# Optimization experiments

Measured on AMD Instinct MI355X. Metric: run time of the kernel, lower is better.

## Reference

```python
import jax, jax.numpy as jnp
import numpy as np

SHAPE = (160, 160, 160)  # spatial grid (D, H, W)
N_VOX = 400_000
C_IN, C_OUT, K = 32, 64, 3


def setup_inputs() -> dict:
    key = jax.random.key(0)
    k1, k2, k3 = jax.random.split(key, 3)
    # unique active voxel coords (batch=0, z, y, x)
    rng = np.random.default_rng(0)
    flat = rng.choice(SHAPE[0] * SHAPE[1] * SHAPE[2], size=N_VOX, replace=False)
    z, y, x = np.unravel_index(flat, SHAPE)
    coors = np.stack([np.zeros(N_VOX, np.int32), z.astype(np.int32), y.astype(np.int32), x.astype(np.int32)], axis=1)
    features = jax.random.normal(k1, (N_VOX, C_IN), dtype=jnp.float32)
    weight = jax.random.normal(k2, (K * K * K, C_IN, C_OUT), dtype=jnp.float32) * (1.0 / np.sqrt(C_IN * K * K * K))
    bias = jax.random.normal(k3, (C_OUT,), dtype=jnp.float32) * 0.01
    return {"features": features, "coors": jnp.asarray(coors), "weight": weight, "bias": bias, "batch_size": 1}


def reference(features, coors, weight, bias, batch_size):
    # Submanifold sparse 3D conv: output coords == input coords.
    n = features.shape[0]
    b, z, y, x = coors[:, 0], coors[:, 1], coors[:, 2], coors[:, 3]
    D, H, W = SHAPE
    # dense voxel->row index lookup grid (the "hash map" for rulebook build)
    grid = jnp.full((batch_size, D, H, W), -1, dtype=jnp.int32)
    grid = grid.at[b, z, y, x].set(jnp.arange(n, dtype=jnp.int32))
    out = jnp.broadcast_to(bias, (n, C_OUT)).astype(features.dtype)
    k = 0
    for dz in (-1, 0, 1):
        for dy in (-1, 0, 1):
            for dx in (-1, 0, 1):
                nz, ny, nx = z + dz, y + dy, x + dx
                inb = (nz >= 0) & (nz < D) & (ny >= 0) & (ny < H) & (nx >= 0) & (nx < W)
                idx = grid[b, jnp.clip(nz, 0, D - 1), jnp.clip(ny, 0, H - 1), jnp.clip(nx, 0, W - 1)]
                valid = inb & (idx >= 0)
                gathered = jnp.where(valid[:, None], features[jnp.clip(idx, 0)], 0.0)  # [n, C_IN]
                out = out + gathered @ weight[k]  # small GEMM per kernel offset
                k += 1
    return out
```

## Files before the change

kernel.cpp:

```cpp
#include <hip/hip_runtime.h>
#include <stdint.h>

#define DD 160
#define HH 160
#define WW 160
#define NGRID (DD*HH*WW)
#define CIN 32
#define COUT 64
#define KK 27
#define BLOCK 1024
#define WPB 16
#define NBLOCKS 256
#define M27 0x07FFFFFFu

typedef _Float16 h2_t __attribute__((ext_vector_type(2)));

__device__ __forceinline__ h2_t as_h2(uint32_t u) {
    union { uint32_t u; h2_t h; } c; c.u = u; return c.h;
}
__device__ __forceinline__ uint32_t f2h(float f) {
    union { _Float16 h; uint16_t u; } c; c.h = (_Float16)f; return (uint32_t)c.u;
}

__device__ __forceinline__ float dot2(uint32_t fu, uint32_t wu, float acc) {
#if defined(__has_builtin)
#if __has_builtin(__builtin_amdgcn_fdot2)
    return __builtin_amdgcn_fdot2(as_h2(fu), as_h2(wu), acc, false);
#else
    h2_t f = as_h2(fu), w = as_h2(wu);
    acc = fmaf((float)f.x, (float)w.x, acc);
    return fmaf((float)f.y, (float)w.y, acc);
#endif
#else
    h2_t f = as_h2(fu), w = as_h2(wu);
    acc = fmaf((float)f.x, (float)w.x, acc);
    return fmaf((float)f.y, (float)w.y, acc);
#endif
}

__global__ void scatter_grid(const int4* __restrict__ coors, int* __restrict__ grid, int n) {
    int i = blockIdx.x * 256 + threadIdx.x;
    if (i < n) {
        int4 c = coors[i];
        grid[(c.y*HH + c.z)*WW + c.w] = i;
    }
}

__global__ void pack_weights(const float* __restrict__ w, uint4* __restrict__ wpk) {
    int t = blockIdx.x * 256 + threadIdx.x;
    if (t >= KK*4*COUT) return;
    int co = t & 63;
    int g  = (t >> 6) & 3;
    int k  = t >> 8;
    const float* base = w + (size_t)k*CIN*COUT + (size_t)(8*g)*COUT + co;
    uint4 r;
    r.x = f2h(base[0*COUT]) | (f2h(base[1*COUT]) << 16);
    r.y = f2h(base[2*COUT]) | (f2h(base[3*COUT]) << 16);
    r.z = f2h(base[4*COUT]) | (f2h(base[5*COUT]) << 16);
    r.w = f2h(base[6*COUT]) | (f2h(base[7*COUT]) << 16);
    wpk[t] = r;
}

__global__ void feats_to_h(const float4* __restrict__ f, uint2* __restrict__ o, int nq) {
    int i = blockIdx.x * 256 + threadIdx.x;
    if (i < nq) {
        float4 v = f[i];
        uint2 r;
        r.x = f2h(v.x) | (f2h(v.y) << 16);
        r.y = f2h(v.z) | (f2h(v.w) << 16);
        o[i] = r;
    }
}

#define LOAD4(D0,D1,D2,D3,kk) { \
    int j_ = __builtin_amdgcn_readlane(nidx, base + (kk)); \
    const uint4* fp_ = fh4 + (size_t)j_ * 4; \
    D0 = fp_[0]; D1 = fp_[1]; D2 = fp_[2]; D3 = fp_[3]; }

#define MAC4(F0,F1,F2,F3,kk) { \
    const uint4* wl_ = wlds + (size_t)(kk)*4*COUT + lane; \
    uint4 w0_ = wl_[0], w1_ = wl_[COUT], w2_ = wl_[2*COUT], w3_ = wl_[3*COUT]; \
    a0 = dot2(F0.x, w0_.x, a0); a1 = dot2(F0.y, w0_.y, a1); \
    a2 = dot2(F0.z, w0_.z, a2); a3 = dot2(F0.w, w0_.w, a3); \
    a0 = dot2(F1.x, w1_.x, a0); a1 = dot2(F1.y, w1_.y, a1); \
    a2 = dot2(F1.z, w1_.z, a2); a3 = dot2(F1.w, w1_.w, a3); \
    a0 = dot2(F2.x, w2_.x, a0); a1 = dot2(F2.y, w2_.y, a1); \
    a2 = dot2(F2.z, w2_.z, a2); a3 = dot2(F2.w, w2_.w, a3); \
    a0 = dot2(F3.x, w3_.x, a0); a1 = dot2(F3.y, w3_.y, a1); \
    a2 = dot2(F3.z, w3_.z, a2); a3 = dot2(F3.w, w3_.w, a3); }

__global__ __launch_bounds__(BLOCK, 4) void sparse_conv(
    const uint4* __restrict__ fh4, const int4* __restrict__ cc,
    const float* __restrict__ bias, const uint4* __restrict__ wpk,
    const int* __restrict__ grid, float* __restrict__ out, int n)
{
    extern __shared__ uint4 wlds[];

    for (int t = threadIdx.x; t < KK*4*COUT; t += BLOCK)
        wlds[t] = wpk[t];
    __syncthreads();

    const int lane = threadIdx.x & 63;
    const int wave = __builtin_amdgcn_readfirstlane((int)(threadIdx.x >> 6));
    const int stride = NBLOCKS * WPB;
    const int pairstep = 2 * stride;

    const float b = bias[lane];
    const int pl = lane & 31;
    const bool prober = pl < KK;
    const int dz = pl / 9 - 1;
    const int dy = (pl / 3) % 3 - 1;
    const int dx = pl % 3 - 1;
    const int hioff = (lane >= 32) ? stride : 0;

    int v = blockIdx.x * WPB + wave;
    int nidx = -1;

    auto probe = [&](int pb) -> int {
        int r = -1;
        int pv = pb + hioff;
        if (prober && pv < n) {
            int4 c = cc[pv];
            int nz = c.y + dz, ny = c.z + dy, nx = c.w + dx;
            if (nz >= 0 && nz < DD && ny >= 0 && ny < HH && nx >= 0 && nx < WW)
                r = grid[(nz*HH + ny)*WW + nx];
        }
        return r;
    };

    auto runvox = [&](uint32_t m, int base, int vo) {
        float a0 = 0.f, a1 = 0.f, a2 = 0.f, a3 = 0.f;
        uint4 A0, A1, A2, A3, B0, B1, B2, B3;
        int kA = __ffs(m) - 1; m &= m - 1;
        LOAD4(A0, A1, A2, A3, kA);
        for (;;) {
            if (!m) { MAC4(A0, A1, A2, A3, kA); break; }
            int kB = __ffs(m) - 1; m &= m - 1;
            LOAD4(B0, B1, B2, B3, kB);
            MAC4(A0, A1, A2, A3, kA);
            if (!m) { MAC4(B0, B1, B2, B3, kB); break; }
            kA = __ffs(m) - 1; m &= m - 1;
            LOAD4(A0, A1, A2, A3, kA);
            MAC4(B0, B1, B2, B3, kB);
        }
        float r = b + ((a0 + a1) + (a2 + a3));
        __builtin_nontemporal_store(r, out + (size_t)vo * COUT + lane);
    };

    nidx = probe(v);

    while (v < n) {
        unsigned long long bal = __ballot(nidx >= 0);
        int nidx_next = probe(v + pairstep);

        uint32_t m0 = (uint32_t)bal & M27;
        uint32_t m1 = (uint32_t)(bal >> 32) & M27;

        {
            int saved = nidx;
            runvox(m0, 0, v);
            int vB = v + stride;
            if (vB < n) runvox(m1, 32, vB);
            nidx = saved;
        }

        v += pairstep;
        nidx = nidx_next;
    }
}

extern "C" void kernel_launch(void* const* d_in, const int* in_sizes, int n_in,
                              void* d_out, int out_size, void* d_ws, size_t ws_size,
                              hipStream_t stream) {
    const float* feats  = (const float*)d_in[0];
    const int*   coors  = (const int*)d_in[1];
    const float* weight = (const float*)d_in[2];
    const float* bias   = (const float*)d_in[3];
    float*       outp   = (float*)d_out;

    const int n = in_sizes[1] / 4;

    int*   grid = (int*)d_ws;
    uint4* wpk  = (uint4*)((char*)d_ws + (size_t)NGRID * sizeof(int));
    uint2* fh   = (uint2*)((char*)d_ws + (size_t)NGRID * sizeof(int)
                           + (size_t)KK * 4 * COUT * sizeof(uint4));

    hipMemsetAsync(grid, 0xFF, (size_t)NGRID * sizeof(int), stream);
    scatter_grid<<<(n + 255) / 256, 256, 0, stream>>>((const int4*)coors, grid, n);

    pack_weights<<<(KK*4*COUT + 255) / 256, 256, 0, stream>>>(weight, wpk);
    feats_to_h<<<(n * CIN / 4 + 255) / 256, 256, 0, stream>>>((const float4*)feats, fh, n * CIN / 4);

    const size_t lds = (size_t)KK * 4 * COUT * sizeof(uint4);
    sparse_conv<<<NBLOCKS, BLOCK, lds, stream>>>((const uint4*)fh, (const int4*)coors,
                                                 bias, wpk, grid, outp, n);
}
```

Before: 319.6 us.

## Bucket voxels into spatial chunks and process per-offset with register-resident weights

Result: slower. 657.5 us (+105.8%).

```diff
diff --git a/kernel.cpp b/kernel.cpp
--- a/kernel.cpp
+++ b/kernel.cpp
@@ -5,13 +5,14 @@
 #define HH 160
 #define WW 160
 #define NGRID (DD*HH*WW)
+#define NCHUNK 4000
+#define CAP 176
 #define CIN 32
 #define COUT 64
 #define KK 27
-#define BLOCK 1024
-#define WPB 16
-#define NBLOCKS 256
-#define M27 0x07FFFFFFu
+#define BLOCK 512
+#define NB 1024
+#define NPACK (KK*4*COUT)
 
 typedef _Float16 h2_t __attribute__((ext_vector_type(2)));
 
@@ -21,7 +22,6 @@
 __device__ __forceinline__ uint32_t f2h(float f) {
     union { _Float16 h; uint16_t u; } c; c.h = (_Float16)f; return (uint32_t)c.u;
 }
-
 __device__ __forceinline__ float dot2(uint32_t fu, uint32_t wu, float acc) {
 #if defined(__has_builtin)
 #if __has_builtin(__builtin_amdgcn_fdot2)
@@ -38,134 +38,132 @@
 #endif
 }
 
-__global__ void scatter_grid(const int4* __restrict__ coors, int* __restrict__ grid, int n) {
+#define MAC16(F0,F1,F2,F3,W0,W1,W2,W3) { \
+    a0 = dot2(F0.x, W0.x, a0); a1 = dot2(F0.y, W0.y, a1); \
+    a2 = dot2(F0.z, W0.z, a2); a3 = dot2(F0.w, W0.w, a3); \
+    a0 = dot2(F1.x, W1.x, a0); a1 = dot2(F1.y, W1.y, a1); \
+    a2 = dot2(F1.z, W1.z, a2); a3 = dot2(F1.w, W1.w, a3); \
+    a0 = dot2(F2.x, W2.x, a0); a1 = dot2(F2.y, W2.y, a1); \
+    a2 = dot2(F2.z, W2.z, a2); a3 = dot2(F2.w, W2.w, a3); \
+    a0 = dot2(F3.x, W3.x, a0); a1 = dot2(F3.y, W3.y, a1); \
+    a2 = dot2(F3.z, W3.z, a2); a3 = dot2(F3.w, W3.w, a3); }
+
+__global__ void prep(const float4* __restrict__ f4, const int4* __restrict__ coors,
+                     const float* __restrict__ wsrc,
+                     int* __restrict__ grid, int* __restrict__ ctr,
+                     uint32_t* __restrict__ pz, int* __restrict__ om,
+                     uint2* __restrict__ fh, uint4* __restrict__ wpk, int n)
+{
     int i = blockIdx.x * 256 + threadIdx.x;
     if (i < n) {
         int4 c = coors[i];
-        grid[(c.y*HH + c.z)*WW + c.w] = i;
+        int cell = (c.y*HH + c.z)*WW + c.w;
+        int ch = cell >> 10;
+        int r = atomicAdd(&ctr[ch], 1);
+        if (r < CAP) {
+            int sp = ch*CAP + r;
+            grid[cell] = sp;
+            om[sp] = i;
+            pz[sp] = ((uint32_t)c.y << 16) | ((uint32_t)c.z << 8) | (uint32_t)c.w;
+            const float4* src = f4 + (size_t)i * 8;
+            uint2* dst = fh + (size_t)sp * 8;
+            #pragma unroll
+            for (int q = 0; q < 8; ++q) {
+                float4 v = src[q];
+                uint2 rr;
+                rr.x = f2h(v.x) | (f2h(v.y) << 16);
+                rr.y = f2h(v.z) | (f2h(v.w) << 16);
+                dst[q] = rr;
+            }
+        }
+    } else if (i < n + NPACK) {
+        int t = i - n;
+        int co = t & 63, g = (t >> 6) & 3, k = t >> 8;
+        const float* base = wsrc + (size_t)k*CIN*COUT + (size_t)(8*g)*COUT + co;
+        uint4 r;
+        r.x = f2h(base[0*COUT]) | (f2h(base[1*COUT]) << 16);
+        r.y = f2h(base[2*COUT]) | (f2h(base[3*COUT]) << 16);
+        r.z = f2h(base[4*COUT]) | (f2h(base[5*COUT]) << 16);
+        r.w = f2h(base[6*COUT]) | (f2h(base[7*COUT]) << 16);
+        wpk[t] = r;
     }
 }
 
-__global__ void pack_weights(const float* __restrict__ w, uint4* __restrict__ wpk) {
-    int t = blockIdx.x * 256 + threadIdx.x;
-    if (t >= KK*4*COUT) return;
-    int co = t & 63;
-    int g  = (t >> 6) & 3;
-    int k  = t >> 8;
-    const float* base = w + (size_t)k*CIN*COUT + (size_t)(8*g)*COUT + co;
-    uint4 r;
-    r.x = f2h(base[0*COUT]) | (f2h(base[1*COUT]) << 16);
-    r.y = f2h(base[2*COUT]) | (f2h(base[3*COUT]) << 16);
-    r.z = f2h(base[4*COUT]) | (f2h(base[5*COUT]) << 16);
-    r.w = f2h(base[6*COUT]) | (f2h(base[7*COUT]) << 16);
-    wpk[t] = r;
-}
-
-__global__ void feats_to_h(const float4* __restrict__ f, uint2* __restrict__ o, int nq) {
-    int i = blockIdx.x * 256 + threadIdx.x;
-    if (i < nq) {
-        float4 v = f[i];
-        uint2 r;
-        r.x = f2h(v.x) | (f2h(v.y) << 16);
-        r.y = f2h(v.z) | (f2h(v.w) << 16);
-        o[i] = r;
-    }
-}
-
-#define LOAD4(D0,D1,D2,D3,kk) { \
-    int j_ = __builtin_amdgcn_readlane(nidx, base + (kk)); \
-    const uint4* fp_ = fh4 + (size_t)j_ * 4; \
-    D0 = fp_[0]; D1 = fp_[1]; D2 = fp_[2]; D3 = fp_[3]; }
-
-#define MAC4(F0,F1,F2,F3,kk) { \
-    const uint4* wl_ = wlds + (size_t)(kk)*4*COUT + lane; \
-    uint4 w0_ = wl_[0], w1_ = wl_[COUT], w2_ = wl_[2*COUT], w3_ = wl_[3*COUT]; \
-    a0 = dot2(F0.x, w0_.x, a0); a1 = dot2(F0.y, w0_.y, a1); \
-    a2 = dot2(F0.z, w0_.z, a2); a3 = dot2(F0.w, w0_.w, a3); \
-    a0 = dot2(F1.x, w1_.x, a0); a1 = dot2(F1.y, w1_.y, a1); \
-    a2 = dot2(F1.z, w1_.z, a2); a3 = dot2(F1.w, w1_.w, a3); \
-    a0 = dot2(F2.x, w2_.x, a0); a1 = dot2(F2.y, w2_.y, a1); \
-    a2 = dot2(F2.z, w2_.z, a2); a3 = dot2(F2.w, w2_.w, a3); \
-    a0 = dot2(F3.x, w3_.x, a0); a1 = dot2(F3.y, w3_.y, a1); \
-    a2 = dot2(F3.z, w3_.z, a2); a3 = dot2(F3.w, w3_.w, a3); }
-
-__global__ __launch_bounds__(BLOCK, 4) void sparse_conv(
-    const uint4* __restrict__ fh4, const int4* __restrict__ cc,
+__global__ __launch_bounds__(BLOCK, 6) void sparse_conv(
+    const uint4* __restrict__ fh4, const uint32_t* __restrict__ pz,
+    const int* __restrict__ om, const int* __restrict__ ctr,
     const float* __restrict__ bias, const uint4* __restrict__ wpk,
-    const int* __restrict__ grid, float* __restrict__ out, int n)
+    const int* __restrict__ grid, float* __restrict__ out)
 {
-    extern __shared__ uint4 wlds[];
-
-    for (int t = threadIdx.x; t < KK*4*COUT; t += BLOCK)
-        wlds[t] = wpk[t];
-    __syncthreads();
+    __shared__ float part[CAP*COUT];
 
     const int lane = threadIdx.x & 63;
-    const int wave = __builtin_amdgcn_readfirstlane((int)(threadIdx.x >> 6));
-    const int stride = NBLOCKS * WPB;
-    const int pairstep = 2 * stride;
+    const int w = __builtin_amdgcn_readfirstlane((int)(threadIdx.x >> 6));
+    const int b = blockIdx.x;
+    const int sw = ((b & 7) << 7) | (b >> 3);
+    const int lo_c = (int)(((long long)sw     * NCHUNK) / NB);
+    const int hi_c = (int)(((long long)(sw+1) * NCHUNK) / NB);
+    const float bi = bias[lane];
 
-    const float b = bias[lane];
-    const int pl = lane & 31;
-    const bool prober = pl < KK;
-    const int dz = pl / 9 - 1;
-    const int dy = (pl / 3) % 3 - 1;
-    const int dx = pl % 3 - 1;
-    const int hioff = (lane >= 32) ? stride : 0;
-
-    int v = blockIdx.x * WPB + wave;
-    int nidx = -1;
-
-    auto probe = [&](int pb) -> int {
-        int r = -1;
-        int pv = pb + hioff;
-        if (prober && pv < n) {
-            int4 c = cc[pv];
-            int nz = c.y + dz, ny = c.z + dy, nx = c.w + dx;
-            if (nz >= 0 && nz < DD && ny >= 0 && ny < HH && nx >= 0 && nx < WW)
-                r = grid[(nz*HH + ny)*WW + nx];
-        }
-        return r;
-    };
-
-    auto runvox = [&](uint32_t m, int base, int vo) {
-        float a0 = 0.f, a1 = 0.f, a2 = 0.f, a3 = 0.f;
-        uint4 A0, A1, A2, A3, B0, B1, B2, B3;
-        int kA = __ffs(m) - 1; m &= m - 1;
-        LOAD4(A0, A1, A2, A3, kA);
-        for (;;) {
-            if (!m) { MAC4(A0, A1, A2, A3, kA); break; }
-            int kB = __ffs(m) - 1; m &= m - 1;
-            LOAD4(B0, B1, B2, B3, kB);
-            MAC4(A0, A1, A2, A3, kA);
-            if (!m) { MAC4(B0, B1, B2, B3, kB); break; }
-            kA = __ffs(m) - 1; m &= m - 1;
-            LOAD4(A0, A1, A2, A3, kA);
-            MAC4(B0, B1, B2, B3, kB);
-        }
-        float r = b + ((a0 + a1) + (a2 + a3));
-        __builtin_nontemporal_store(r, out + (size_t)vo * COUT + lane);
-    };
-
-    nidx = probe(v);
-
-    while (v < n) {
-        unsigned long long bal = __ballot(nidx >= 0);
-        int nidx_next = probe(v + pairstep);
-
-        uint32_t m0 = (uint32_t)bal & M27;
-        uint32_t m1 = (uint32_t)(bal >> 32) & M27;
+    for (int c = lo_c; c < hi_c; ++c) {
+        int m = ctr[c];
+        if (m > CAP) m = CAP;
+        if (m == 0) continue;
+        const int sp0 = c * CAP;
 
         {
-            int saved = nidx;
-            runvox(m0, 0, v);
-            int vB = v + stride;
-            if (vB < n) runvox(m1, 32, vB);
-            nidx = saved;
+            uint4 W0 = wpk[(13*4+0)*64 + lane], W1 = wpk[(13*4+1)*64 + lane];
+            uint4 W2 = wpk[(13*4+2)*64 + lane], W3 = wpk[(13*4+3)*64 + lane];
+            for (int r = w; r < m; r += 8) {
+                const uint4* fp = fh4 + (size_t)(sp0 + r) * 4;
+                uint4 F0 = fp[0], F1 = fp[1], F2 = fp[2], F3 = fp[3];
+                float a0 = 0.f, a1 = 0.f, a2 = 0.f, a3 = 0.f;
+                MAC16(F0, F1, F2, F3, W0, W1, W2, W3);
+                part[r*64 + lane] = bi + ((a0 + a1) + (a2 + a3));
+            }
         }
+        __syncthreads();
 
-        v += pairstep;
-        nidx = nidx_next;
+        for (int li = w; li < 26; li += 8) {
+            const int k = li + (li >= 13 ? 1 : 0);
+            uint4 W0 = wpk[(k*4+0)*64 + lane], W1 = wpk[(k*4+1)*64 + lane];
+            uint4 W2 = wpk[(k*4+2)*64 + lane], W3 = wpk[(k*4+3)*64 + lane];
+            int t9 = (k*57) >> 9;  int r9 = k - t9*9;
+            int t3 = (r9*171) >> 9;
+            const int dz = t9 - 1, dy = t3 - 1, dx = (r9 - t3*3) - 1;
+
+            for (int r0 = 0; r0 < m; r0 += 64) {
+                int r = r0 + lane;
+                int nidx = -1;
+                if (r < m) {
+                    uint32_t p = pz[sp0 + r];
+                    int z = (int)(p >> 16) + dz;
+                    int y = (int)((p >> 8) & 255) + dy;
+                    int x = (int)(p & 255) + dx;
+                    if (z >= 0 && z < DD && y >= 0 && y < HH && x >= 0 && x < WW)
+                        nidx = grid[(z*HH + y)*WW + x];
+                }
+                unsigned long long bal = __ballot(nidx >= 0);
+                while (bal) {
+                    int bpos = __builtin_ctzll(bal);
+                    bal &= bal - 1;
+                    int j = __builtin_amdgcn_readlane(nidx, bpos);
+                    const uint4* fp = fh4 + (size_t)j * 4;
+                    uint4 F0 = fp[0], F1 = fp[1], F2 = fp[2], F3 = fp[3];
+                    float a0 = 0.f, a1 = 0.f, a2 = 0.f, a3 = 0.f;
+                    MAC16(F0, F1, F2, F3, W0, W1, W2, W3);
+                    unsafeAtomicAdd(&part[(r0 + bpos)*64 + lane], (a0 + a1) + (a2 + a3));
+                }
+            }
+        }
+        __syncthreads();
+
+        for (int r = w; r < m; r += 8) {
+            float val = part[r*64 + lane];
+            int orig = om[sp0 + r];
+            __builtin_nontemporal_store(val, out + (size_t)orig * COUT + lane);
+        }
+        __syncthreads();
     }
 }
 
@@ -180,18 +178,21 @@
 
     const int n = in_sizes[1] / 4;
 
-    int*   grid = (int*)d_ws;
-    uint4* wpk  = (uint4*)((char*)d_ws + (size_t)NGRID * sizeof(int));
-    uint2* fh   = (uint2*)((char*)d_ws + (size_t)NGRID * sizeof(int)
-                           + (size_t)KK * 4 * COUT * sizeof(uint4));
+    char* ws = (char*)d_ws;
+    int*      grid = (int*)ws;        ws += (size_t)NGRID * 4;
+    int*      ctr  = (int*)ws;        ws += 16384;
+    uint4*    wpk  = (uint4*)ws;      ws += (size_t)NPACK * 16;
+    uint32_t* pz   = (uint32_t*)ws;   ws += (size_t)NCHUNK * CAP * 4;
+    int*      om   = (int*)ws;        ws += (size_t)NCHUNK * CAP * 4;
+    uint2*    fh   = (uint2*)ws;
 
-    hipMemsetAsync(grid, 0xFF, (size_t)NGRID * sizeof(int), stream);
-    scatter_grid<<<(n + 255) / 256, 256, 0, stream>>>((const int4*)coors, grid, n);
+    hipMemsetAsync(grid, 0xFF, (size_t)NGRID * 4, stream);
+    hipMemsetAsync(ctr, 0, 16384, stream);
 
-    pack_weights<<<(KK*4*COUT + 255) / 256, 256, 0, stream>>>(weight, wpk);
-    feats_to_h<<<(n * CIN / 4 + 255) / 256, 256, 0, stream>>>((const float4*)feats, fh, n * CIN / 4);
+    prep<<<(n + NPACK + 255) / 256, 256, 0, stream>>>(
+        (const float4*)feats, (const int4*)coors, weight,
+        grid, ctr, pz, om, fh, wpk, n);
 
-    const size_t lds = (size_t)KK * 4 * COUT * sizeof(uint4);
-    sparse_conv<<<NBLOCKS, BLOCK, lds, stream>>>((const uint4*)fh, (const int4*)coors,
-                                                 bias, wpk, grid, outp, n);
+    sparse_conv<<<NB, BLOCK, 0, stream>>>((const uint4*)fh, pz, om, ctr,
+                                          bias, wpk, grid, outp);
 }
```
